# Optimization experiments

Hardware: AMD Instinct MI355X
Metric: run time of the kernel (lower is better)

## Reference

```python
import jax, jax.numpy as jnp
import numpy as np
import math

B, S, D, H = 2, 2048, 1024, 16
HD = D // H  # head dim = 64


def setup_inputs() -> dict:
    key = jax.random.key(0)
    ks = jax.random.split(key, 8)
    scale = 1.0 / math.sqrt(D)
    return {
        "x": jax.random.normal(ks[0], (B, S, D), dtype=jnp.float32),
        "mask": jax.random.randint(ks[1], (B, S, S), 0, 2).astype(bool),
        "Wq": jax.random.normal(ks[2], (D, D), dtype=jnp.float32) * scale,
        "bq": jax.random.normal(ks[3], (D,), dtype=jnp.float32) * 0.01,
        "Wk": jax.random.normal(ks[4], (D, D), dtype=jnp.float32) * scale,
        "bk": jax.random.normal(ks[5], (D,), dtype=jnp.float32) * 0.01,
        "Wv": jax.random.normal(ks[6], (D, D), dtype=jnp.float32) * scale,
        "bv": jax.random.normal(ks[7], (D,), dtype=jnp.float32) * 0.01,
    }


def reference(x, mask, Wq, bq, Wk, bk, Wv, bv):
    # Linear projections (weights stored as [in, out])
    q = x @ Wq + bq  # [B,S,D]
    k = x @ Wk + bk
    v = x @ Wv + bv
    # split heads -> [B,H,S,HD]
    q = q.reshape(B, S, H, HD).transpose(0, 2, 1, 3)
    k = k.reshape(B, S, H, HD).transpose(0, 2, 1, 3)
    v = v.reshape(B, S, H, HD).transpose(0, 2, 1, 3)
    scores = jnp.einsum("bhqd,bhkd->bhqk", q, k) / jnp.sqrt(jnp.float32(HD))
    # Faithful to the source: masked_fill_(mask, -inf) is immediately
    # overwritten by masked_fill_(mask, 0), so masked positions end up 0
    # BEFORE the softmax (a quirk of the original module).
    scores = jnp.where(mask[:, None, :, :], 0.0, scores)
    attn = jax.nn.softmax(scores, axis=-1)  # dropout=0.0 (eval)
    out = jnp.einsum("bhqk,bhkd->bhqd", attn, v)
    return out.transpose(0, 2, 1, 3).reshape(B, S, D)
```

## Files before the change

kernel.cpp:

```cpp
#include <hip/hip_runtime.h>
#include <cstdint>
#include <cstddef>

static constexpr int B_ = 2, S_ = 2048, D_ = 1024, H_ = 16, HD_ = 64;

typedef float f32x4 __attribute__((ext_vector_type(4)));
typedef short bf16x8 __attribute__((ext_vector_type(8)));

__device__ __forceinline__ unsigned short f2bf(float f) {
    union { float f; unsigned int u; } v; v.f = f;
    unsigned int r = v.u + 0x7FFFu + ((v.u >> 16) & 1u);
    return (unsigned short)(r >> 16);
}

__device__ __forceinline__ unsigned pack2bf(float a, float b) {
    union { float f; unsigned u; } va, vb; va.f = a; vb.f = b;
    unsigned ra = va.u + 0x7FFFu + ((va.u >> 16) & 1u);
    unsigned rb = vb.u + 0x7FFFu + ((vb.u >> 16) & 1u);
    return __builtin_amdgcn_perm(rb, ra, 0x07060302u);
}

__device__ __forceinline__ void gload_lds16(const void* g, void* l) {
    __builtin_amdgcn_global_load_lds(
        (const __attribute__((address_space(1))) void*)g,
        (__attribute__((address_space(3))) void*)l, 16, 0, 0);
}

__global__ __launch_bounds__(256)
void prep(const float* __restrict__ x, unsigned short* __restrict__ xo,
          const int* __restrict__ m, unsigned char* __restrict__ mo,
          const float* __restrict__ Wq, const float* __restrict__ Wk,
          const float* __restrict__ Wv, unsigned short* __restrict__ wt) {
    __shared__ unsigned short Ts[64][72];
    const int bid = blockIdx.x, t = threadIdx.x;
    if (bid < 2048) {
        size_t i = ((size_t)bid * 256 + t) * 8;
        float4 a = *(const float4*)(x + i);
        float4 c = *(const float4*)(x + i + 4);
        uint4 r;
        r.x = pack2bf(a.x, a.y); r.y = pack2bf(a.z, a.w);
        r.z = pack2bf(c.x, c.y); r.w = pack2bf(c.z, c.w);
        *(uint4*)(xo + i) = r;
    } else if (bid < 4096) {
        size_t i = ((size_t)(bid - 2048) * 256 + t) * 16;
        uint4 r;
        unsigned w[4];
        #pragma unroll
        for (int g = 0; g < 4; ++g) {
            int4 v = *(const int4*)(m + i + g * 4);
            w[g] = (v.x ? 0xFFu : 0u) | (v.y ? 0xFF00u : 0u) |
                   (v.z ? 0xFF0000u : 0u) | (v.w ? 0xFF000000u : 0u);
        }
        r.x = w[0]; r.y = w[1]; r.z = w[2]; r.w = w[3];
        *(uint4*)(mo + i) = r;
    } else {
        const int tid = bid - 4096;
        const int mat = tid >> 8, tile = tid & 255;
        const float* __restrict__ W = (mat == 0) ? Wq : (mat == 1) ? Wk : Wv;
        unsigned short* __restrict__ o = wt + (size_t)mat * D_ * D_;
        const int n0 = (tile & 15) * 64, k0 = (tile >> 4) * 64;
        {
            const int nl = t & 63, kb = t >> 6;
            #pragma unroll
            for (int i = 0; i < 16; ++i) {
                int k = kb + i * 4;
                Ts[nl][k] = f2bf(W[(size_t)(k0 + k) * D_ + n0 + nl]);
            }
        }
        __syncthreads();
        {
            const int kl = t & 63, nb = t >> 6;
            #pragma unroll
            for (int i = 0; i < 16; ++i) {
                int n = nb + i * 4;
                o[(size_t)(n0 + n) * D_ + k0 + kl] = Ts[n][kl];
            }
        }
    }
}

__global__ __launch_bounds__(512)
void qkv_gemm(const unsigned short* __restrict__ xb, const unsigned short* __restrict__ wt,
              const float* __restrict__ bq, const float* __restrict__ bk,
              const float* __restrict__ bv,
              unsigned short* __restrict__ qo, unsigned short* __restrict__ ko,
              unsigned short* __restrict__ vto) {
    const int bx = blockIdx.x;
    const int by = blockIdx.y;
    const int mat = bx >> 3;
    const int ncol0 = (bx & 7) * 128;
    const float* __restrict__ bias = (mat == 0) ? bq : (mat == 1) ? bk : bv;
    const unsigned short* __restrict__ Wm = wt + (size_t)mat * D_ * D_;

    __shared__ unsigned short As[2][128 * 32];
    __shared__ unsigned short Bs[2][128 * 32];

    const int t = threadIdx.x;
    const int w = t >> 6, lane = t & 63;
    const int l15 = lane & 15, quad = lane >> 4;
    const int mw = (w >> 2) * 64, nw = (w & 3) * 32;
    const int rowBase = by * 128;

    const int r16 = lane >> 2;
    const int sslot = lane & 3;
    const int sg = (sslot ^ ((r16 >> 1) & 3)) * 8;
    const int srow = w * 16 + r16;
    const int rcol = (quad ^ ((l15 >> 1) & 3)) * 8;

    f32x4 acc[4][2] = {};

    gload_lds16(xb + (size_t)(rowBase + srow) * D_ + sg, &As[0][w * 16 * 32]);
    gload_lds16(Wm + (size_t)(ncol0 + srow) * D_ + sg, &Bs[0][w * 16 * 32]);

    for (int it = 0; it < 32; ++it) {
        const int cur = it & 1;
        __syncthreads();
        if (it + 1 < 32) {
            const int ktn = (it + 1) * 32;
            gload_lds16(xb + (size_t)(rowBase + srow) * D_ + ktn + sg,
                        &As[cur ^ 1][w * 16 * 32]);
            gload_lds16(Wm + (size_t)(ncol0 + srow) * D_ + ktn + sg,
                        &Bs[cur ^ 1][w * 16 * 32]);
        }

        bf16x8 a[4], b[2];
        #pragma unroll
        for (int i = 0; i < 4; ++i)
            a[i] = *(const bf16x8*)&As[cur][(mw + i * 16 + l15) * 32 + rcol];
        #pragma unroll
        for (int j = 0; j < 2; ++j)
            b[j] = *(const bf16x8*)&Bs[cur][(nw + j * 16 + l15) * 32 + rcol];
        #pragma unroll
        for (int i = 0; i < 4; ++i)
            #pragma unroll
            for (int j = 0; j < 2; ++j)
                acc[i][j] = __builtin_amdgcn_mfma_f32_16x16x32_bf16(a[i], b[j], acc[i][j], 0, 0, 0);
    }

    if (mat < 2) {
        unsigned short* __restrict__ O = (mat == 0) ? qo : ko;
        const float osc = (mat == 0) ? 0.18033688011112443f : 1.0f;
        #pragma unroll
        for (int j = 0; j < 2; ++j) {
            const int col = ncol0 + nw + j * 16 + l15;
            const float bb = bias[col];
            #pragma unroll
            for (int i = 0; i < 4; ++i)
                #pragma unroll
                for (int r = 0; r < 4; ++r) {
                    const int m = rowBase + mw + i * 16 + quad * 4 + r;
                    O[(size_t)m * D_ + col] = f2bf((acc[i][j][r] + bb) * osc);
                }
        }
    } else {
        #pragma unroll
        for (int j = 0; j < 2; ++j) {
            const int col = ncol0 + nw + j * 16 + l15;
            const float bb = bias[col];
            const int hh = col >> 6, hd = col & 63;
            #pragma unroll
            for (int i = 0; i < 4; ++i) {
                const int m0 = rowBase + mw + i * 16 + quad * 4;
                const int bg = m0 >> 11, s0 = m0 & 2047;
                ushort4 pk;
                pk.x = f2bf(acc[i][j][0] + bb);
                pk.y = f2bf(acc[i][j][1] + bb);
                pk.z = f2bf(acc[i][j][2] + bb);
                pk.w = f2bf(acc[i][j][3] + bb);
                *(ushort4*)&vto[(((size_t)bg * H_ + hh) * HD_ + hd) * S_ + s0] = pk;
            }
        }
    }
}

__global__ __launch_bounds__(512, 4)
void attn_mfma(const unsigned short* __restrict__ qmat,
               const unsigned short* __restrict__ kmat,
               const unsigned short* __restrict__ vtg,
               const unsigned char* __restrict__ msk, float* __restrict__ out) {
    const int h = blockIdx.x, qt = blockIdx.y, b = blockIdx.z;
    const int t = threadIdx.x, w = t >> 6, lane = t & 63;
    const int l15 = lane & 15, quad = lane >> 4;
    const int q0 = qt * 128;

    __shared__ unsigned short Ks[2][64 * 64];
    __shared__ unsigned short Vs[2][64 * 64];
    __shared__ __align__(16) unsigned short Ps[128 * 64];

    const size_t bh = (size_t)b * S_ * D_ + (size_t)h * HD_;
    const unsigned short* __restrict__ qp = qmat + bh;
    const unsigned short* __restrict__ kp = kmat + bh;
    const unsigned short* __restrict__ vp = vtg + ((size_t)b * H_ + h) * HD_ * S_;
    const unsigned char* __restrict__ mb = msk + (size_t)b * S_ * S_;

    const int rs = lane >> 3, sslot = lane & 7;
    const int sg = (sslot ^ rs) * 8;
    const int srow = w * 8 + rs;

    const int qr = w * 16 + l15;
    const int sw7 = l15 & 7;

    bf16x8 qfr[2];
    #pragma unroll
    for (int kst = 0; kst < 2; ++kst)
        qfr[kst] = *(const bf16x8*)(qp + (size_t)(q0 + qr) * D_ + kst * 32 + quad * 8);

    f32x4 accO[4] = {};
    f32x4 lsA = {};
    bf16x8 ones;
    #pragma unroll
    for (int i = 0; i < 8; ++i) ones[i] = (short)0x3F80;

    gload_lds16(kp + (size_t)srow * D_ + sg, &Ks[0][w * 8 * 64]);
    gload_lds16(vp + (size_t)srow * S_ + sg, &Vs[0][w * 8 * 64]);

    for (int it = 0; it < 32; ++it) {
        const int cur = it & 1;
        const int kt = it * 64;
        __syncthreads();

        unsigned mu[4];
        {
            const unsigned char* __restrict__ mrow = mb + (size_t)(q0 + qr) * S_ + kt;
            #pragma unroll
            for (int mt = 0; mt < 4; ++mt)
                mu[mt] = *(const unsigned*)(mrow + mt * 16 + quad * 4);
        }

        if (it + 1 < 32) {
            const int ktn = kt + 64;
            gload_lds16(kp + (size_t)(ktn + srow) * D_ + sg, &Ks[cur ^ 1][w * 8 * 64]);
            gload_lds16(vp + (size_t)srow * S_ + ktn + sg, &Vs[cur ^ 1][w * 8 * 64]);
        }

        f32x4 sc[4] = {};
        #pragma unroll
        for (int kst = 0; kst < 2; ++kst) {
            bf16x8 kfr[4];
            #pragma unroll
            for (int mt = 0; mt < 4; ++mt) {
                const int R = mt * 16 + l15;
                kfr[mt] = *(const bf16x8*)&Ks[cur][R * 64 + (((kst * 4 + quad) ^ sw7) * 8)];
            }
            __builtin_amdgcn_s_setprio(1);
            #pragma unroll
            for (int mt = 0; mt < 4; ++mt)
                sc[mt] = __builtin_amdgcn_mfma_f32_16x16x32_bf16(kfr[mt], qfr[kst], sc[mt], 0, 0, 0);
            __builtin_amdgcn_s_setprio(0);
        }

        #pragma unroll
        for (int mt = 0; mt < 4; ++mt) {
            unsigned p0 = pack2bf(__builtin_amdgcn_exp2f(sc[mt][0]),
                                  __builtin_amdgcn_exp2f(sc[mt][1]));
            unsigned p1 = pack2bf(__builtin_amdgcn_exp2f(sc[mt][2]),
                                  __builtin_amdgcn_exp2f(sc[mt][3]));
            const unsigned m0 = __builtin_amdgcn_perm(0u, mu[mt], 0x01010000u);
            const unsigned m1 = __builtin_amdgcn_perm(0u, mu[mt], 0x03030202u);
            p0 = (m0 & 0x3F803F80u) | (~m0 & p0);
            p1 = (m1 & 0x3F803F80u) | (~m1 & p1);
            uint2 pk2; pk2.x = p0; pk2.y = p1;
            *(uint2*)((char*)Ps + qr * 128 +
                      (((2 * mt + (quad >> 1)) ^ sw7) * 16) + (quad & 1) * 8) = pk2;
        }

        #pragma unroll
        for (int kst = 0; kst < 2; ++kst) {
            bf16x8 vfr[4];
            #pragma unroll
            for (int dt = 0; dt < 4; ++dt) {
                const int R = dt * 16 + l15;
                vfr[dt] = *(const bf16x8*)&Vs[cur][R * 64 + (((kst * 4 + quad) ^ sw7) * 8)];
            }
            bf16x8 pfr = *(const bf16x8*)((const char*)Ps + qr * 128 +
                                          (((kst * 4 + quad) ^ sw7) * 16));
            __builtin_amdgcn_s_setprio(1);
            #pragma unroll
            for (int dt = 0; dt < 4; ++dt)
                accO[dt] = __builtin_amdgcn_mfma_f32_16x16x32_bf16(pfr, vfr[dt], accO[dt], 0, 0, 0);
            lsA = __builtin_amdgcn_mfma_f32_16x16x32_bf16(pfr, ones, lsA, 0, 0, 0);
            __builtin_amdgcn_s_setprio(0);
        }
    }

    float* __restrict__ ob = out + ((size_t)b * S_ + q0) * D_ + (size_t)h * HD_;
    #pragma unroll
    for (int r = 0; r < 4; ++r) {
        const float inv = 1.0f / lsA[r];
        const int row = w * 16 + quad * 4 + r;
        #pragma unroll
        for (int dt = 0; dt < 4; ++dt)
            ob[(size_t)row * D_ + dt * 16 + l15] = accO[dt][r] * inv;
    }
}

extern "C" void kernel_launch(void* const* d_in, const int* in_sizes, int n_in,
                              void* d_out, int out_size, void* d_ws, size_t ws_size,
                              hipStream_t stream) {
    (void)in_sizes; (void)n_in; (void)out_size; (void)ws_size;
    const float* x    = (const float*)d_in[0];
    const int*   mask = (const int*)d_in[1];
    const float* Wq   = (const float*)d_in[2];
    const float* bq   = (const float*)d_in[3];
    const float* Wk   = (const float*)d_in[4];
    const float* bk   = (const float*)d_in[5];
    const float* Wv   = (const float*)d_in[6];
    const float* bv   = (const float*)d_in[7];
    float* out = (float*)d_out;

    const size_t M1 = (size_t)1024 * 1024;
    unsigned short* xb  = (unsigned short*)d_ws;
    unsigned short* wtb = xb + 4 * M1;
    unsigned short* qb  = wtb + 3 * M1;
    unsigned short* kb  = qb + 4 * M1;
    unsigned short* vtb = kb + 4 * M1;
    unsigned char*  mk  = (unsigned char*)(vtb + 4 * M1);

    prep<<<4864, 256, 0, stream>>>(x, xb, mask, mk, Wq, Wk, Wv, wtb);
    qkv_gemm<<<dim3(24, 32), 512, 0, stream>>>(xb, wtb, bq, bk, bv, qb, kb, vtb);
    attn_mfma<<<dim3(16, 16, 2), 512, 0, stream>>>(qb, kb, vtb, mk, out);
}
```

Measured before the change: 208.4 us.

## Split attention KV tile across wave pairs with 1024-thread blocks and LDS reduction

Doubles the attention block to 16 waves. Each pair of waves shares 16 query rows, and each wave of the pair handles half of each 64-key tile for QK^T and half of the contraction for PV. Half of the waves stage the K tile and the other half stage the V tile. Partial output and row-sum accumulators are combined through LDS at the end. The aim is more parallelism and latency hiding per CU at the cost of a final reduction, per-wave register limits from the tighter launch bounds, and fewer MFMAs per wave between barriers.

```diff
diff --git a/kernel.cpp b/kernel.cpp
--- a/kernel.cpp
+++ b/kernel.cpp
@@ -173,7 +173,7 @@
     }
 }
 
-__global__ __launch_bounds__(512, 4)
+__global__ __launch_bounds__(1024, 8)
 void attn_mfma(const unsigned short* __restrict__ qmat,
                const unsigned short* __restrict__ kmat,
                const unsigned short* __restrict__ vtg,
@@ -183,9 +183,10 @@
     const int l15 = lane & 15, quad = lane >> 4;
     const int q0 = qt * 128;
 
-    __shared__ unsigned short Ks[2][64 * 64];
-    __shared__ unsigned short Vs[2][64 * 64];
-    __shared__ __align__(16) unsigned short Ps[128 * 64];
+    __shared__ __align__(16) char smem[49152];
+    unsigned short* const Ksm = (unsigned short*)smem;
+    unsigned short* const Vsm = (unsigned short*)(smem + 16384);
+    unsigned short* const Psm = (unsigned short*)(smem + 32768);
 
     const size_t bh = (size_t)b * S_ * D_ + (size_t)h * HD_;
     const unsigned short* __restrict__ qp = qmat + bh;
@@ -195,9 +196,12 @@
 
     const int rs = lane >> 3, sslot = lane & 7;
     const int sg = (sslot ^ rs) * 8;
-    const int srow = w * 8 + rs;
-
-    const int qr = w * 16 + l15;
+    const int sr8 = (w & 7) * 8 + rs;
+    const bool stK = (w < 8);
+
+    const int wq = w >> 1;
+    const int kw = (w & 1) * 32;
+    const int qr = wq * 16 + l15;
     const int sw7 = l15 & 7;
 
     bf16x8 qfr[2];
@@ -211,46 +215,49 @@
     #pragma unroll
     for (int i = 0; i < 8; ++i) ones[i] = (short)0x3F80;
 
-    gload_lds16(kp + (size_t)srow * D_ + sg, &Ks[0][w * 8 * 64]);
-    gload_lds16(vp + (size_t)srow * S_ + sg, &Vs[0][w * 8 * 64]);
+    if (stK) gload_lds16(kp + (size_t)sr8 * D_ + sg, Ksm + (w & 7) * 8 * 64);
+    else     gload_lds16(vp + (size_t)sr8 * S_ + sg, Vsm + (w & 7) * 8 * 64);
 
     for (int it = 0; it < 32; ++it) {
         const int cur = it & 1;
         const int kt = it * 64;
         __syncthreads();
 
-        unsigned mu[4];
+        unsigned mu[2];
         {
-            const unsigned char* __restrict__ mrow = mb + (size_t)(q0 + qr) * S_ + kt;
-            #pragma unroll
-            for (int mt = 0; mt < 4; ++mt)
-                mu[mt] = *(const unsigned*)(mrow + mt * 16 + quad * 4);
+            const unsigned char* __restrict__ mrow = mb + (size_t)(q0 + qr) * S_ + kt + kw;
+            mu[0] = *(const unsigned*)(mrow + quad * 4);
+            mu[1] = *(const unsigned*)(mrow + 16 + quad * 4);
         }
 
         if (it + 1 < 32) {
             const int ktn = kt + 64;
-            gload_lds16(kp + (size_t)(ktn + srow) * D_ + sg, &Ks[cur ^ 1][w * 8 * 64]);
-            gload_lds16(vp + (size_t)srow * S_ + ktn + sg, &Vs[cur ^ 1][w * 8 * 64]);
-        }
-
-        f32x4 sc[4] = {};
+            if (stK) gload_lds16(kp + (size_t)(ktn + sr8) * D_ + sg,
+                                 Ksm + (cur ^ 1) * 4096 + (w & 7) * 8 * 64);
+            else     gload_lds16(vp + (size_t)sr8 * S_ + ktn + sg,
+                                 Vsm + (cur ^ 1) * 4096 + (w & 7) * 8 * 64);
+        }
+
+        f32x4 sc[2] = {};
         #pragma unroll
         for (int kst = 0; kst < 2; ++kst) {
-            bf16x8 kfr[4];
-            #pragma unroll
-            for (int mt = 0; mt < 4; ++mt) {
-                const int R = mt * 16 + l15;
-                kfr[mt] = *(const bf16x8*)&Ks[cur][R * 64 + (((kst * 4 + quad) ^ sw7) * 8)];
+            bf16x8 kfr[2];
+            #pragma unroll
+            for (int mt = 0; mt < 2; ++mt) {
+                const int R = kw + mt * 16 + l15;
+                kfr[mt] = *(const bf16x8*)&Ksm[cur * 4096 + R * 64 +
+                                               (((kst * 4 + quad) ^ sw7) * 8)];
             }
             __builtin_amdgcn_s_setprio(1);
             #pragma unroll
-            for (int mt = 0; mt < 4; ++mt)
+            for (int mt = 0; mt < 2; ++mt)
                 sc[mt] = __builtin_amdgcn_mfma_f32_16x16x32_bf16(kfr[mt], qfr[kst], sc[mt], 0, 0, 0);
             __builtin_amdgcn_s_setprio(0);
         }
 
         #pragma unroll
-        for (int mt = 0; mt < 4; ++mt) {
+        for (int mt = 0; mt < 2; ++mt) {
+            const int mtg = (w & 1) * 2 + mt;
             unsigned p0 = pack2bf(__builtin_amdgcn_exp2f(sc[mt][0]),
                                   __builtin_amdgcn_exp2f(sc[mt][1]));
             unsigned p1 = pack2bf(__builtin_amdgcn_exp2f(sc[mt][2]),
@@ -260,19 +267,20 @@
             p0 = (m0 & 0x3F803F80u) | (~m0 & p0);
             p1 = (m1 & 0x3F803F80u) | (~m1 & p1);
             uint2 pk2; pk2.x = p0; pk2.y = p1;
-            *(uint2*)((char*)Ps + qr * 128 +
-                      (((2 * mt + (quad >> 1)) ^ sw7) * 16) + (quad & 1) * 8) = pk2;
-        }
-
-        #pragma unroll
-        for (int kst = 0; kst < 2; ++kst) {
+            *(uint2*)((char*)Psm + qr * 128 +
+                      (((2 * mtg + (quad >> 1)) ^ sw7) * 16) + (quad & 1) * 8) = pk2;
+        }
+
+        {
+            const int kst = w & 1;
             bf16x8 vfr[4];
             #pragma unroll
             for (int dt = 0; dt < 4; ++dt) {
                 const int R = dt * 16 + l15;
-                vfr[dt] = *(const bf16x8*)&Vs[cur][R * 64 + (((kst * 4 + quad) ^ sw7) * 8)];
-            }
-            bf16x8 pfr = *(const bf16x8*)((const char*)Ps + qr * 128 +
+                vfr[dt] = *(const bf16x8*)&Vsm[cur * 4096 + R * 64 +
+                                               (((kst * 4 + quad) ^ sw7) * 8)];
+            }
+            bf16x8 pfr = *(const bf16x8*)((const char*)Psm + qr * 128 +
                                           (((kst * 4 + quad) ^ sw7) * 16));
             __builtin_amdgcn_s_setprio(1);
             #pragma unroll
@@ -283,14 +291,31 @@
         }
     }
 
-    float* __restrict__ ob = out + ((size_t)b * S_ + q0) * D_ + (size_t)h * HD_;
-    #pragma unroll
-    for (int r = 0; r < 4; ++r) {
-        const float inv = 1.0f / lsA[r];
-        const int row = w * 16 + quad * 4 + r;
+    __syncthreads();
+    float* const Red = (float*)smem;
+    const int pidx = (wq * 64 + lane) * 20;
+    if (w & 1) {
         #pragma unroll
         for (int dt = 0; dt < 4; ++dt)
-            ob[(size_t)row * D_ + dt * 16 + l15] = accO[dt][r] * inv;
+            *(f32x4*)&Red[pidx + dt * 4] = accO[dt];
+        *(f32x4*)&Red[pidx + 16] = lsA;
+    }
+    __syncthreads();
+    if (!(w & 1)) {
+        #pragma unroll
+        for (int dt = 0; dt < 4; ++dt)
+            accO[dt] += *(const f32x4*)&Red[pidx + dt * 4];
+        lsA += *(const f32x4*)&Red[pidx + 16];
+
+        float* __restrict__ ob = out + ((size_t)b * S_ + q0) * D_ + (size_t)h * HD_;
+        #pragma unroll
+        for (int r = 0; r < 4; ++r) {
+            const float inv = 1.0f / lsA[r];
+            const int row = wq * 16 + quad * 4 + r;
+            #pragma unroll
+            for (int dt = 0; dt < 4; ++dt)
+                ob[(size_t)row * D_ + dt * 16 + l15] = accO[dt][r] * inv;
+        }
     }
 }
 
@@ -318,5 +343,5 @@
 
     prep<<<4864, 256, 0, stream>>>(x, xb, mask, mk, Wq, Wk, Wv, wtb);
     qkv_gemm<<<dim3(24, 32), 512, 0, stream>>>(xb, wtb, bq, bk, bv, qb, kb, vtb);
-    attn_mfma<<<dim3(16, 16, 2), 512, 0, stream>>>(qb, kb, vtb, mk, out);
-}
+    attn_mfma<<<dim3(16, 16, 2), 1024, 0, stream>>>(qb, kb, vtb, mk, out);
+}
```

Measured after the change: 257.4 us. +23.5%, slower.
